# Kernel tuning notes

Measured on AMD Instinct MI355X. Metric: run time of the kernel, lower is better.

The kernel has to match this reference:

```python
import jax, jax.numpy as jnp
import numpy as np

B, N = 4, 1024
D_MODEL, N_HEADS, D_HEAD, D_COORD = 512, 8, 64, 2


def setup_inputs() -> dict:
    key = jax.random.key(0)
    ks = jax.random.split(key, 8)
    sd = 1.0 / np.sqrt(D_MODEL)
    return {
        "x": jax.random.normal(ks[0], (B, N, D_MODEL), dtype=jnp.float32),
        "positions": jax.random.uniform(ks[1], (N, D_COORD), dtype=jnp.float32) * 32.0,
        "W_Q": jax.random.normal(ks[2], (D_MODEL, N_HEADS * D_HEAD), dtype=jnp.float32) * sd,
        "W_K": jax.random.normal(ks[3], (D_MODEL, N_HEADS * D_HEAD), dtype=jnp.float32) * sd,
        "W_V": jax.random.normal(ks[4], (D_MODEL, N_HEADS * D_HEAD), dtype=jnp.float32) * sd,
        "W_O": jax.random.normal(ks[5], (N_HEADS * D_HEAD, D_MODEL), dtype=jnp.float32) * sd,
        "U": jax.random.normal(ks[6], (N_HEADS, D_HEAD, D_HEAD), dtype=jnp.float32),
        "freqs": jax.random.normal(ks[7], (N_HEADS, D_HEAD // 2, D_COORD), dtype=jnp.float32),
    }


def reference(x, positions, W_Q, W_K, W_V, W_O, U, freqs):
    # x: (B,N,d_model); positions: (N,d_coord); U: (H,dh,dh); freqs: (H,m,d_coord)
    Bn, Nn, _ = x.shape
    H, dh, _ = U.shape
    m = dh // 2
    scale = (dh // 2) ** -0.5

    Q = (x @ W_Q).reshape(Bn, Nn, H, dh)
    K = (x @ W_K).reshape(Bn, Nn, H, dh)
    V = (x @ W_V).reshape(Bn, Nn, H, dh)

    # Active-subspace projector: Pi = qr(U)[0] @ qr(U)[0].T per head
    Uq = jax.vmap(lambda u: jnp.linalg.qr(u)[0])(U)              # (H,dh,dh)
    P = jnp.einsum('hde,hfe->hdf', Uq, Uq)                       # U U^T
    Qp = jnp.einsum('bnhd,hdf->bhnf', Q, P)                      # (B,H,N,dh)
    Kp = jnp.einsum('bnhd,hdf->bhnf', K, P)

    # Relative rotation: R_rel(r_j - r_i) is block-diag 2x2 rotations with
    # angle theta_ijm = freqs_m . (r_j - r_i) = a_jm - a_im (separable), so
    # q^T R(r_j-r_i) k = (R(a_i)q)^T (R(a_j)k)  -- exact RoPE identity.
    ang = jnp.einsum('nc,hmc->hnm', positions, freqs)            # (H,N,m)
    c = jnp.cos(ang)[None]                                       # (1,H,N,m)
    s = jnp.sin(ang)[None]

    def rot(v):  # v: (B,H,N,dh) -> rotated (even, odd) halves (B,H,N,m)
        ve, vo = v[..., ::2], v[..., 1::2]
        return ve * c - vo * s, ve * s + vo * c

    qe, qo = rot(Qp)
    ke, ko = rot(Kp)
    scores = (jnp.einsum('bhim,bhjm->bhij', qe, ke)
              + jnp.einsum('bhim,bhjm->bhij', qo, ko)) * scale   # (B,H,N,N)
    w = jax.nn.softmax(scores, axis=-1)
    out = jnp.einsum('bhij,bjhd->bihd', w, V).reshape(Bn, Nn, H * dh)
    return out @ W_O
```

## Files before the change

### kernel.cpp

```cpp
#include <hip/hip_runtime.h>
#include <hip/hip_bf16.h>
#include <math.h>

#define NBATCH 4
#define NSEQ   1024
#define DMODEL 512
#define NH     8
#define DH     64
#define MROWS  (NBATCH*NSEQ)
#define MHALF  (DH/2)

typedef __attribute__((ext_vector_type(8))) short bf16x8;
typedef __attribute__((ext_vector_type(4))) float floatx4;

__device__ __forceinline__ uint f2bf2(float lo, float hi) {
    union { __hip_bfloat162 h; uint u; } v;
    v.h = __float22bfloat162_rn(make_float2(lo, hi));
    return v.u;
}

__global__ __launch_bounds__(256) void prep_kernel(
    const float* __restrict__ pos, const float* __restrict__ freqs,
    const float* __restrict__ x,
    const float* __restrict__ Wq, const float* __restrict__ Wk,
    const float* __restrict__ Wv, const float* __restrict__ Wo,
    float* __restrict__ cosT, float* __restrict__ sinT,
    ushort* __restrict__ xb, ushort* __restrict__ Wt)
{
    __shared__ float T[64][65];
    const int bid = blockIdx.x;
    const int tid = threadIdx.x;

    if (bid < 1024) {
        int idx = bid * 256 + tid;
        int m = idx & 31;
        int n = (idx >> 5) & 1023;
        int h = idx >> 15;
        float a = pos[n*2+0] * freqs[(h*MHALF+m)*2+0]
                + pos[n*2+1] * freqs[(h*MHALF+m)*2+1];
        cosT[idx] = cosf(a);
        sinT[idx] = sinf(a);
    } else if (bid < 2048) {
        int idx = ((bid - 1024) * 256 + tid) * 8;
        float4 a = *(const float4*)&x[idx];
        float4 b = *(const float4*)&x[idx+4];
        uint4 pk;
        pk.x = f2bf2(a.x, a.y);
        pk.y = f2bf2(a.z, a.w);
        pk.z = f2bf2(b.x, b.y);
        pk.w = f2bf2(b.z, b.w);
        *(uint4*)&xb[idx] = pk;
    } else {
        int b2 = bid - 2048;
        int n0g = (b2 & 31) * 64;
        int k0  = (b2 >> 5) * 64;
        int mat = n0g >> 9;
        const float* W = (mat == 0) ? Wq : ((mat == 1) ? Wk : ((mat == 2) ? Wv : Wo));
        int n0 = n0g & 511;
        int c = tid & 63, r = tid >> 6;
        #pragma unroll
        for (int i = 0; i < 16; i++)
            T[r + i*4][c] = W[(k0 + r + i*4) * DMODEL + n0 + c];
        __syncthreads();
        int nl = tid >> 2;
        int kg = tid & 3;
        #pragma unroll
        for (int g = 0; g < 4; g++) {
            int kl = kg * 16 + g * 4;
            uint2 pk;
            pk.x = f2bf2(T[kl+0][nl], T[kl+1][nl]);
            pk.y = f2bf2(T[kl+2][nl], T[kl+3][nl]);
            *(uint2*)&Wt[(size_t)(n0g + nl) * DMODEL + k0 + kl] = pk;
        }
    }
}

__global__ __launch_bounds__(256) void qkv_gemm(
    const ushort* __restrict__ xb, const ushort* __restrict__ Wt,
    const float* __restrict__ cosT, const float* __restrict__ sinT,
    ushort* __restrict__ Qb, ushort* __restrict__ Kb, ushort* __restrict__ Vt)
{
    __shared__ __align__(16) ushort AB[2 * 64 * 72];
    ushort* As = AB;
    ushort* Bs = AB + 64 * 72;
    float (*Cs)[65] = (float(*)[65])AB;

    const int cb = blockIdx.x;
    const int rb = blockIdx.y;
    const int mat = cb >> 3;
    const int c0 = (cb & 7) * 64;
    const int r0 = rb * 64;
    const int ng0 = mat * 512 + c0;

    const int tid = threadIdx.x;
    const int w = tid >> 6, l = tid & 63;
    const int lr = l & 15, lg = l >> 4;

    const int srow = tid >> 2;
    const int scol = (tid & 3) * 16;

    floatx4 acc[4];
    #pragma unroll
    for (int nt = 0; nt < 4; nt++) acc[nt] = (floatx4){0.f,0.f,0.f,0.f};

    const ushort* pa = &xb[(size_t)(r0 + srow) * DMODEL + scol];
    const ushort* pb = &Wt[(size_t)(ng0 + srow) * DMODEL + scol];
    uint4 ra0 = *(const uint4*)pa;
    uint4 ra1 = *(const uint4*)(pa + 8);
    uint4 rb0 = *(const uint4*)pb;
    uint4 rb1 = *(const uint4*)(pb + 8);

    for (int k0 = 0; k0 < DMODEL; k0 += 64) {
        __syncthreads();
        *(uint4*)&As[srow*72 + scol]     = ra0;
        *(uint4*)&As[srow*72 + scol + 8] = ra1;
        *(uint4*)&Bs[srow*72 + scol]     = rb0;
        *(uint4*)&Bs[srow*72 + scol + 8] = rb1;
        __syncthreads();

        if (k0 + 64 < DMODEL) {
            const ushort* na = &xb[(size_t)(r0 + srow) * DMODEL + k0 + 64 + scol];
            const ushort* nb = &Wt[(size_t)(ng0 + srow) * DMODEL + k0 + 64 + scol];
            ra0 = *(const uint4*)na;
            ra1 = *(const uint4*)(na + 8);
            rb0 = *(const uint4*)nb;
            rb1 = *(const uint4*)(nb + 8);
        }

        #pragma unroll
        for (int ks = 0; ks < 2; ks++) {
            bf16x8 af = *(const bf16x8*)&As[(16*w + lr)*72 + ks*32 + lg*8];
            #pragma unroll
            for (int nt = 0; nt < 4; nt++) {
                bf16x8 bf = *(const bf16x8*)&Bs[(nt*16 + lr)*72 + ks*32 + lg*8];
                acc[nt] = __builtin_amdgcn_mfma_f32_16x16x32_bf16(af, bf, acc[nt], 0, 0, 0);
            }
        }
    }

    __syncthreads();
    #pragma unroll
    for (int nt = 0; nt < 4; nt++)
        #pragma unroll
        for (int r = 0; r < 4; r++)
            Cs[16*w + lg*4 + r][nt*16 + lr] = acc[nt][r];
    __syncthreads();

    const int tx = tid & 15, ty = tid >> 4;
    const int dbase = tx * 4;
    const int head = c0 >> 6;

    if (mat == 2) {
        int rowbase = r0 + ty * 4;
        int b = rowbase >> 10, n0 = rowbase & 1023;
        size_t vbase = (size_t)(b * NH + head) * DH;
        #pragma unroll
        for (int j = 0; j < 4; j++) {
            uint2 pk;
            pk.x = f2bf2(Cs[ty*4 + 0][tx*4 + j], Cs[ty*4 + 1][tx*4 + j]);
            pk.y = f2bf2(Cs[ty*4 + 2][tx*4 + j], Cs[ty*4 + 3][tx*4 + j]);
            *(uint2*)&Vt[(vbase + dbase + j) * NSEQ + n0] = pk;
        }
    } else {
        ushort* dst = (mat == 0) ? Qb : Kb;
        const float qs2 = (mat == 0) ? 0.17677669529663687f : 1.0f;
        #pragma unroll
        for (int i = 0; i < 4; i++) {
            int row = r0 + ty * 4 + i;
            int b = row >> 10, n = row & 1023;
            float v[4];
            #pragma unroll
            for (int p = 0; p < 2; p++) {
                int de = dbase + 2 * p;
                int m = de >> 1;
                float c = cosT[(head * NSEQ + n) * MHALF + m] * qs2;
                float s = sinT[(head * NSEQ + n) * MHALF + m] * qs2;
                float ve = Cs[ty*4 + i][tx*4 + 2*p];
                float vo = Cs[ty*4 + i][tx*4 + 2*p + 1];
                v[2*p]     = ve * c - vo * s;
                v[2*p + 1] = ve * s + vo * c;
            }
            uint2 pk;
            pk.x = f2bf2(v[0], v[1]);
            pk.y = f2bf2(v[2], v[3]);
            *(uint2*)&dst[((size_t)(b * NH + head) * NSEQ + n) * DH + dbase] = pk;
        }
    }
}

__global__ __launch_bounds__(256, 4) void attn_kernel(
    const ushort* __restrict__ Qb, const ushort* __restrict__ Kb,
    const ushort* __restrict__ Vt, ushort* __restrict__ Obb)
{
    __shared__ __align__(16) ushort S[2*64*72 + 32*72];
    ushort* Ks = S;
    ushort* Vs = S + 64*72;
    ushort* Ps = S + 2*64*72;

    const int tid = threadIdx.x;
    const int w = tid >> 6, l = tid & 63;
    const int lr = l & 15, lg = l >> 4;
    const int qs = w & 1;
    const int jh = w >> 1;
    const int bh = blockIdx.y, q0 = blockIdx.x * 32;

    const ushort* Qg = Qb + (size_t)bh * NSEQ * DH;
    const ushort* Kg = Kb + (size_t)bh * NSEQ * DH;
    const ushort* Vg = Vt + (size_t)bh * DH * NSEQ;

    bf16x8 qf[2];
    #pragma unroll
    for (int ks = 0; ks < 2; ks++)
        qf[ks] = *(const bf16x8*)(Qg + (size_t)(q0 + 16*qs + lr) * DH + ks*32 + lg*8);

    floatx4 ot[4];
    #pragma unroll
    for (int i = 0; i < 4; i++) ot[i] = (floatx4){0.f, 0.f, 0.f, 0.f};
    float l_lane = 0.f;

    const int sr = tid >> 2;
    const int sc = (tid & 3) * 16;

    const ushort* kp = Kg + (size_t)sr * DH + sc;
    uint4 ka  = *(const uint4*)kp;
    uint4 kb2 = *(const uint4*)(kp + 8);
    const ushort* vp = Vg + (size_t)sr * NSEQ + sc;
    uint4 va  = *(const uint4*)vp;
    uint4 vb2 = *(const uint4*)(vp + 8);

    for (int jt = 0; jt < 16; jt++) {
        __syncthreads();
        *(uint4*)&Ks[sr*72 + sc]     = ka;
        *(uint4*)&Ks[sr*72 + sc + 8] = kb2;
        *(uint4*)&Vs[sr*72 + sc]     = va;
        *(uint4*)&Vs[sr*72 + sc + 8] = vb2;
        __syncthreads();

        if (jt < 15) {
            const ushort* kn = Kg + (size_t)((jt+1)*64 + sr) * DH + sc;
            ka  = *(const uint4*)kn;
            kb2 = *(const uint4*)(kn + 8);
            const ushort* vn = Vg + (size_t)sr * NSEQ + (jt+1)*64 + sc;
            va  = *(const uint4*)vn;
            vb2 = *(const uint4*)(vn + 8);
        }

        #pragma unroll
        for (int jm2 = 0; jm2 < 2; jm2++) {
            const int jm = jh*2 + jm2;
            floatx4 acc = (floatx4){0.f, 0.f, 0.f, 0.f};
            #pragma unroll
            for (int ks = 0; ks < 2; ks++) {
                bf16x8 af = *(const bf16x8*)&Ks[(jm*16 + lr)*72 + ks*32 + lg*8];
                acc = __builtin_amdgcn_mfma_f32_16x16x32_bf16(af, qf[ks], acc, 0, 0, 0);
            }
            float p0 = __expf(acc[0]);
            float p1 = __expf(acc[1]);
            float p2 = __expf(acc[2]);
            float p3 = __expf(acc[3]);
            l_lane += (p0 + p1) + (p2 + p3);
            uint2 pk;
            pk.x = f2bf2(p0, p1);
            pk.y = f2bf2(p2, p3);
            *(uint2*)&Ps[(16*qs + lr)*72 + jm*16 + lg*4] = pk;
        }

        {
            bf16x8 pf = *(const bf16x8*)&Ps[(16*qs + lr)*72 + jh*32 + lg*8];
            #pragma unroll
            for (int dt = 0; dt < 4; dt++) {
                bf16x8 af = *(const bf16x8*)&Vs[(dt*16 + lr)*72 + jh*32 + lg*8];
                ot[dt] = __builtin_amdgcn_mfma_f32_16x16x32_bf16(af, pf, ot[dt], 0, 0, 0);
            }
        }
    }

    l_lane += __shfl_xor(l_lane, 16, 64);
    l_lane += __shfl_xor(l_lane, 32, 64);

    __syncthreads();
    float* Os = (float*)S;
    float* Ls = (float*)(S + 5120);
    if (w >= 2) {
        #pragma unroll
        for (int dt = 0; dt < 4; dt++)
            *(float4*)&Os[(qs*64 + l)*20 + dt*4] = *(float4*)&ot[dt];
        if (lg == 0) Ls[qs*16 + lr] = l_lane;
    }
    __syncthreads();
    if (w < 2) {
        float lsum = l_lane + Ls[qs*16 + lr];
        float inv = 1.f / lsum;
        int n = q0 + 16*qs + lr;
        size_t obase = ((size_t)bh * NSEQ + n) * DH;
        #pragma unroll
        for (int dt = 0; dt < 4; dt++) {
            float4 p = *(const float4*)&Os[(qs*64 + l)*20 + dt*4];
            uint2 pk;
            pk.x = f2bf2((ot[dt][0] + p.x) * inv, (ot[dt][1] + p.y) * inv);
            pk.y = f2bf2((ot[dt][2] + p.z) * inv, (ot[dt][3] + p.w) * inv);
            *(uint2*)&Obb[obase + dt*16 + lg*4] = pk;
        }
    }
}

__global__ __launch_bounds__(256) void out_gemm(
    const ushort* __restrict__ Obb, const ushort* __restrict__ Wt,
    float* __restrict__ out)
{
    __shared__ ushort As[64 * 40];
    __shared__ ushort Bs[64 * 40];
    __shared__ float  Cs[64][65];

    const int cb = blockIdx.x;
    const int rb = blockIdx.y;
    const int c0 = cb * 64, r0 = rb * 64;

    const int tid = threadIdx.x;
    const int w = tid >> 6, l = tid & 63;
    const int lr = l & 15, lg = l >> 4;
    const int srow = tid >> 2;
    const int sgrp = tid & 3;

    const int arow = r0 + srow;
    const int b = arow >> 10, n = arow & 1023;

    floatx4 acc[4];
    #pragma unroll
    for (int nt = 0; nt < 4; nt++) acc[nt] = (floatx4){0.f,0.f,0.f,0.f};

    #define A_ADDR(K0) (&Obb[((size_t)(b*NH + ((K0) >> 6)) * NSEQ + n) * DH + ((K0) & 63) + sgrp*8])

    uint4 rav = *(const uint4*)A_ADDR(0);
    uint4 rbv = *(const uint4*)&Wt[(size_t)(1536 + c0 + srow) * DMODEL + sgrp*8];

    for (int k0 = 0; k0 < DMODEL; k0 += 32) {
        __syncthreads();
        *(uint4*)&As[srow*40 + sgrp*8] = rav;
        *(uint4*)&Bs[srow*40 + sgrp*8] = rbv;
        __syncthreads();

        if (k0 + 32 < DMODEL) {
            rav = *(const uint4*)A_ADDR(k0 + 32);
            rbv = *(const uint4*)&Wt[(size_t)(1536 + c0 + srow) * DMODEL + (k0 + 32) + sgrp*8];
        }

        bf16x8 af = *(const bf16x8*)&As[(16*w + lr)*40 + lg*8];
        #pragma unroll
        for (int nt = 0; nt < 4; nt++) {
            bf16x8 bf = *(const bf16x8*)&Bs[(nt*16 + lr)*40 + lg*8];
            acc[nt] = __builtin_amdgcn_mfma_f32_16x16x32_bf16(af, bf, acc[nt], 0, 0, 0);
        }
    }
    #undef A_ADDR

    __syncthreads();
    #pragma unroll
    for (int nt = 0; nt < 4; nt++)
        #pragma unroll
        for (int r = 0; r < 4; r++)
            Cs[16*w + lg*4 + r][nt*16 + lr] = acc[nt][r];
    __syncthreads();

    const int tx = tid & 15, ty = tid >> 4;
    #pragma unroll
    for (int i = 0; i < 4; i++) {
        float4 o;
        o.x = Cs[ty*4 + i][tx*4 + 0];
        o.y = Cs[ty*4 + i][tx*4 + 1];
        o.z = Cs[ty*4 + i][tx*4 + 2];
        o.w = Cs[ty*4 + i][tx*4 + 3];
        *(float4*)&out[(size_t)(r0 + ty*4 + i) * DMODEL + c0 + tx*4] = o;
    }
}

extern "C" void kernel_launch(void* const* d_in, const int* in_sizes, int n_in,
                              void* d_out, int out_size, void* d_ws, size_t ws_size,
                              hipStream_t stream) {
    const float* x         = (const float*)d_in[0];
    const float* positions = (const float*)d_in[1];
    const float* Wq        = (const float*)d_in[2];
    const float* Wk        = (const float*)d_in[3];
    const float* Wv        = (const float*)d_in[4];
    const float* Wo        = (const float*)d_in[5];
    const float* freqs     = (const float*)d_in[7];
    float* out = (float*)d_out;

    float*  ws    = (float*)d_ws;
    float*  cosT  = ws;
    float*  sinT  = cosT + NH*NSEQ*MHALF;
    ushort* xb    = (ushort*)(sinT + NH*NSEQ*MHALF);
    ushort* Wt    = xb + (size_t)MROWS*DMODEL;
    ushort* Qb    = Wt + (size_t)2048*DMODEL;
    ushort* Kb    = Qb + (size_t)NBATCH*NH*NSEQ*DH;
    ushort* Vt    = Kb + (size_t)NBATCH*NH*NSEQ*DH;
    ushort* Obb   = Vt + (size_t)NBATCH*NH*NSEQ*DH;

    prep_kernel<<<dim3(2304), 256, 0, stream>>>(positions, freqs, x, Wq, Wk, Wv, Wo,
                                                cosT, sinT, xb, Wt);
    qkv_gemm<<<dim3(24, 64), 256, 0, stream>>>(xb, Wt, cosT, sinT, Qb, Kb, Vt);
    attn_kernel<<<dim3(32, 32), 256, 0, stream>>>(Qb, Kb, Vt, Obb);
    out_gemm<<<dim3(8, 64), 256, 0, stream>>>(Obb, Wt, out);
}
```

Baseline: 123.0 us.

## Double query rows per attention block to reuse K/V tiles

The attention kernel now processes 64 query rows per block instead of 32. Each wave handles two 16-row query groups, so every K and V fragment read from shared memory feeds two MFMAs. The grid is halved, and launch bounds drop to 2 blocks per SM to allow more registers. The intent is to halve the global and LDS traffic for K/V per query. The trade-off is higher register pressure and only 512 blocks, which lowers occupancy and parallelism.

```diff
diff --git a/kernel.cpp b/kernel.cpp
--- a/kernel.cpp
+++ b/kernel.cpp
@@ -188,11 +188,11 @@
     }
 }
 
-__global__ __launch_bounds__(256, 4) void attn_kernel(
+__global__ __launch_bounds__(256, 2) void attn_kernel(
     const ushort* __restrict__ Qb, const ushort* __restrict__ Kb,
     const ushort* __restrict__ Vt, ushort* __restrict__ Obb)
 {
-    __shared__ __align__(16) ushort S[2*64*72 + 32*72];
+    __shared__ __align__(16) ushort S[3 * 64 * 72];
     ushort* Ks = S;
     ushort* Vs = S + 64*72;
     ushort* Ps = S + 2*64*72;
@@ -200,23 +200,24 @@
     const int tid = threadIdx.x;
     const int w = tid >> 6, l = tid & 63;
     const int lr = l & 15, lg = l >> 4;
-    const int qs = w & 1;
+    const int qh = w & 1;
     const int jh = w >> 1;
-    const int bh = blockIdx.y, q0 = blockIdx.x * 32;
+    const int bh = blockIdx.y, q0 = blockIdx.x * 64;
 
     const ushort* Qg = Qb + (size_t)bh * NSEQ * DH;
     const ushort* Kg = Kb + (size_t)bh * NSEQ * DH;
     const ushort* Vg = Vt + (size_t)bh * DH * NSEQ;
 
-    bf16x8 qf[2];
-    #pragma unroll
-    for (int ks = 0; ks < 2; ks++)
-        qf[ks] = *(const bf16x8*)(Qg + (size_t)(q0 + 16*qs + lr) * DH + ks*32 + lg*8);
-
-    floatx4 ot[4];
-    #pragma unroll
-    for (int i = 0; i < 4; i++) ot[i] = (floatx4){0.f, 0.f, 0.f, 0.f};
-    float l_lane = 0.f;
+    const int qrA = q0 + 32*qh + lr;
+    const int qrB = qrA + 16;
+    bf16x8 qfA0 = *(const bf16x8*)(Qg + (size_t)qrA * DH + lg*8);
+    bf16x8 qfA1 = *(const bf16x8*)(Qg + (size_t)qrA * DH + 32 + lg*8);
+    bf16x8 qfB0 = *(const bf16x8*)(Qg + (size_t)qrB * DH + lg*8);
+    bf16x8 qfB1 = *(const bf16x8*)(Qg + (size_t)qrB * DH + 32 + lg*8);
+
+    floatx4 otA0 = (floatx4){0.f,0.f,0.f,0.f}, otA1 = otA0, otA2 = otA0, otA3 = otA0;
+    floatx4 otB0 = otA0, otB1 = otA0, otB2 = otA0, otB3 = otA0;
+    float lA = 0.f, lB = 0.f;
 
     const int sr = tid >> 2;
     const int sc = (tid & 3) * 16;
@@ -248,59 +249,116 @@
         #pragma unroll
         for (int jm2 = 0; jm2 < 2; jm2++) {
             const int jm = jh*2 + jm2;
-            floatx4 acc = (floatx4){0.f, 0.f, 0.f, 0.f};
-            #pragma unroll
-            for (int ks = 0; ks < 2; ks++) {
-                bf16x8 af = *(const bf16x8*)&Ks[(jm*16 + lr)*72 + ks*32 + lg*8];
-                acc = __builtin_amdgcn_mfma_f32_16x16x32_bf16(af, qf[ks], acc, 0, 0, 0);
-            }
-            float p0 = __expf(acc[0]);
-            float p1 = __expf(acc[1]);
-            float p2 = __expf(acc[2]);
-            float p3 = __expf(acc[3]);
-            l_lane += (p0 + p1) + (p2 + p3);
-            uint2 pk;
-            pk.x = f2bf2(p0, p1);
-            pk.y = f2bf2(p2, p3);
-            *(uint2*)&Ps[(16*qs + lr)*72 + jm*16 + lg*4] = pk;
+            bf16x8 af0 = *(const bf16x8*)&Ks[(jm*16 + lr)*72 + lg*8];
+            bf16x8 af1 = *(const bf16x8*)&Ks[(jm*16 + lr)*72 + 32 + lg*8];
+            floatx4 accA = (floatx4){0.f,0.f,0.f,0.f};
+            floatx4 accB = (floatx4){0.f,0.f,0.f,0.f};
+            accA = __builtin_amdgcn_mfma_f32_16x16x32_bf16(af0, qfA0, accA, 0, 0, 0);
+            accA = __builtin_amdgcn_mfma_f32_16x16x32_bf16(af1, qfA1, accA, 0, 0, 0);
+            accB = __builtin_amdgcn_mfma_f32_16x16x32_bf16(af0, qfB0, accB, 0, 0, 0);
+            accB = __builtin_amdgcn_mfma_f32_16x16x32_bf16(af1, qfB1, accB, 0, 0, 0);
+
+            float a0 = __expf(accA[0]);
+            float a1 = __expf(accA[1]);
+            float a2 = __expf(accA[2]);
+            float a3 = __expf(accA[3]);
+            lA += (a0 + a1) + (a2 + a3);
+            uint2 pkA;
+            pkA.x = f2bf2(a0, a1);
+            pkA.y = f2bf2(a2, a3);
+            *(uint2*)&Ps[(32*qh + lr)*72 + jm*16 + lg*4] = pkA;
+
+            float b0 = __expf(accB[0]);
+            float b1 = __expf(accB[1]);
+            float b2 = __expf(accB[2]);
+            float b3 = __expf(accB[3]);
+            lB += (b0 + b1) + (b2 + b3);
+            uint2 pkB;
+            pkB.x = f2bf2(b0, b1);
+            pkB.y = f2bf2(b2, b3);
+            *(uint2*)&Ps[(32*qh + 16 + lr)*72 + jm*16 + lg*4] = pkB;
         }
 
         {
-            bf16x8 pf = *(const bf16x8*)&Ps[(16*qs + lr)*72 + jh*32 + lg*8];
-            #pragma unroll
-            for (int dt = 0; dt < 4; dt++) {
-                bf16x8 af = *(const bf16x8*)&Vs[(dt*16 + lr)*72 + jh*32 + lg*8];
-                ot[dt] = __builtin_amdgcn_mfma_f32_16x16x32_bf16(af, pf, ot[dt], 0, 0, 0);
-            }
-        }
-    }
-
-    l_lane += __shfl_xor(l_lane, 16, 64);
-    l_lane += __shfl_xor(l_lane, 32, 64);
+            bf16x8 pfA = *(const bf16x8*)&Ps[(32*qh + lr)*72 + jh*32 + lg*8];
+            bf16x8 pfB = *(const bf16x8*)&Ps[(32*qh + 16 + lr)*72 + jh*32 + lg*8];
+            bf16x8 af;
+            af = *(const bf16x8*)&Vs[(0*16 + lr)*72 + jh*32 + lg*8];
+            otA0 = __builtin_amdgcn_mfma_f32_16x16x32_bf16(af, pfA, otA0, 0, 0, 0);
+            otB0 = __builtin_amdgcn_mfma_f32_16x16x32_bf16(af, pfB, otB0, 0, 0, 0);
+            af = *(const bf16x8*)&Vs[(1*16 + lr)*72 + jh*32 + lg*8];
+            otA1 = __builtin_amdgcn_mfma_f32_16x16x32_bf16(af, pfA, otA1, 0, 0, 0);
+            otB1 = __builtin_amdgcn_mfma_f32_16x16x32_bf16(af, pfB, otB1, 0, 0, 0);
+            af = *(const bf16x8*)&Vs[(2*16 + lr)*72 + jh*32 + lg*8];
+            otA2 = __builtin_amdgcn_mfma_f32_16x16x32_bf16(af, pfA, otA2, 0, 0, 0);
+            otB2 = __builtin_amdgcn_mfma_f32_16x16x32_bf16(af, pfB, otB2, 0, 0, 0);
+            af = *(const bf16x8*)&Vs[(3*16 + lr)*72 + jh*32 + lg*8];
+            otA3 = __builtin_amdgcn_mfma_f32_16x16x32_bf16(af, pfA, otA3, 0, 0, 0);
+            otB3 = __builtin_amdgcn_mfma_f32_16x16x32_bf16(af, pfB, otB3, 0, 0, 0);
+        }
+    }
+
+    lA += __shfl_xor(lA, 16, 64);
+    lA += __shfl_xor(lA, 32, 64);
+    lB += __shfl_xor(lB, 16, 64);
+    lB += __shfl_xor(lB, 32, 64);
 
     __syncthreads();
     float* Os = (float*)S;
-    float* Ls = (float*)(S + 5120);
-    if (w >= 2) {
-        #pragma unroll
-        for (int dt = 0; dt < 4; dt++)
-            *(float4*)&Os[(qs*64 + l)*20 + dt*4] = *(float4*)&ot[dt];
-        if (lg == 0) Ls[qs*16 + lr] = l_lane;
-    }
-    __syncthreads();
-    if (w < 2) {
-        float lsum = l_lane + Ls[qs*16 + lr];
-        float inv = 1.f / lsum;
-        int n = q0 + 16*qs + lr;
-        size_t obase = ((size_t)bh * NSEQ + n) * DH;
-        #pragma unroll
-        for (int dt = 0; dt < 4; dt++) {
-            float4 p = *(const float4*)&Os[(qs*64 + l)*20 + dt*4];
-            uint2 pk;
-            pk.x = f2bf2((ot[dt][0] + p.x) * inv, (ot[dt][1] + p.y) * inv);
-            pk.y = f2bf2((ot[dt][2] + p.z) * inv, (ot[dt][3] + p.w) * inv);
-            *(uint2*)&Obb[obase + dt*16 + lg*4] = pk;
-        }
+    float* Ls = (float*)(S + 8704);
+    const int qlA = 32*qh + lr;
+    const int qlB = qlA + 16;
+    if (jh == 1) {
+        *(float4*)&Os[qlA*68 + 0*16 + lg*4] = *(float4*)&otA0;
+        *(float4*)&Os[qlA*68 + 1*16 + lg*4] = *(float4*)&otA1;
+        *(float4*)&Os[qlA*68 + 2*16 + lg*4] = *(float4*)&otA2;
+        *(float4*)&Os[qlA*68 + 3*16 + lg*4] = *(float4*)&otA3;
+        *(float4*)&Os[qlB*68 + 0*16 + lg*4] = *(float4*)&otB0;
+        *(float4*)&Os[qlB*68 + 1*16 + lg*4] = *(float4*)&otB1;
+        *(float4*)&Os[qlB*68 + 2*16 + lg*4] = *(float4*)&otB2;
+        *(float4*)&Os[qlB*68 + 3*16 + lg*4] = *(float4*)&otB3;
+        if (lg == 0) { Ls[qlA] = lA; Ls[qlB] = lB; }
+    }
+    __syncthreads();
+    if (jh == 0) {
+        float invA = 1.f / (lA + Ls[qlA]);
+        float invB = 1.f / (lB + Ls[qlB]);
+        size_t obA = ((size_t)bh * NSEQ + q0 + qlA) * DH;
+        size_t obB = ((size_t)bh * NSEQ + q0 + qlB) * DH;
+        float4 p;
+        uint2 pk;
+        p = *(const float4*)&Os[qlA*68 + 0*16 + lg*4];
+        pk.x = f2bf2((otA0[0] + p.x) * invA, (otA0[1] + p.y) * invA);
+        pk.y = f2bf2((otA0[2] + p.z) * invA, (otA0[3] + p.w) * invA);
+        *(uint2*)&Obb[obA + 0*16 + lg*4] = pk;
+        p = *(const float4*)&Os[qlA*68 + 1*16 + lg*4];
+        pk.x = f2bf2((otA1[0] + p.x) * invA, (otA1[1] + p.y) * invA);
+        pk.y = f2bf2((otA1[2] + p.z) * invA, (otA1[3] + p.w) * invA);
+        *(uint2*)&Obb[obA + 1*16 + lg*4] = pk;
+        p = *(const float4*)&Os[qlA*68 + 2*16 + lg*4];
+        pk.x = f2bf2((otA2[0] + p.x) * invA, (otA2[1] + p.y) * invA);
+        pk.y = f2bf2((otA2[2] + p.z) * invA, (otA2[3] + p.w) * invA);
+        *(uint2*)&Obb[obA + 2*16 + lg*4] = pk;
+        p = *(const float4*)&Os[qlA*68 + 3*16 + lg*4];
+        pk.x = f2bf2((otA3[0] + p.x) * invA, (otA3[1] + p.y) * invA);
+        pk.y = f2bf2((otA3[2] + p.z) * invA, (otA3[3] + p.w) * invA);
+        *(uint2*)&Obb[obA + 3*16 + lg*4] = pk;
+        p = *(const float4*)&Os[qlB*68 + 0*16 + lg*4];
+        pk.x = f2bf2((otB0[0] + p.x) * invB, (otB0[1] + p.y) * invB);
+        pk.y = f2bf2((otB0[2] + p.z) * invB, (otB0[3] + p.w) * invB);
+        *(uint2*)&Obb[obB + 0*16 + lg*4] = pk;
+        p = *(const float4*)&Os[qlB*68 + 1*16 + lg*4];
+        pk.x = f2bf2((otB1[0] + p.x) * invB, (otB1[1] + p.y) * invB);
+        pk.y = f2bf2((otB1[2] + p.z) * invB, (otB1[3] + p.w) * invB);
+        *(uint2*)&Obb[obB + 1*16 + lg*4] = pk;
+        p = *(const float4*)&Os[qlB*68 + 2*16 + lg*4];
+        pk.x = f2bf2((otB2[0] + p.x) * invB, (otB2[1] + p.y) * invB);
+        pk.y = f2bf2((otB2[2] + p.z) * invB, (otB2[3] + p.w) * invB);
+        *(uint2*)&Obb[obB + 2*16 + lg*4] = pk;
+        p = *(const float4*)&Os[qlB*68 + 3*16 + lg*4];
+        pk.x = f2bf2((otB3[0] + p.x) * invB, (otB3[1] + p.y) * invB);
+        pk.y = f2bf2((otB3[2] + p.z) * invB, (otB3[3] + p.w) * invB);
+        *(uint2*)&Obb[obB + 3*16 + lg*4] = pk;
     }
 }
 
@@ -399,6 +457,6 @@
     prep_kernel<<<dim3(2304), 256, 0, stream>>>(positions, freqs, x, Wq, Wk, Wv, Wo,
                                                 cosT, sinT, xb, Wt);
     qkv_gemm<<<dim3(24, 64), 256, 0, stream>>>(xb, Wt, cosT, sinT, Qb, Kb, Vt);
-    attn_kernel<<<dim3(32, 32), 256, 0, stream>>>(Qb, Kb, Vt, Obb);
+    attn_kernel<<<dim3(16, 32), 256, 0, stream>>>(Qb, Kb, Vt, Obb);
     out_gemm<<<dim3(8, 64), 256, 0, stream>>>(Obb, Wt, out);
 }
```

New measurement: 125.3 us. Within noise of the previous version (+1.8%).
